# Performance work log

Measured on AMD Instinct MI355X. Metric: run time of the kernel, lower is better.

Reference implementation:

```python
import jax, jax.numpy as jnp
import numpy as np

BETA = 10.0    # ste surrogate-gradient scale (module default beta=10)
SLOPE = 1.0
GAMMA = 100.0  # trigger sharpness (module default gamma=100)
EPS = 1e-30

# Straight-through estimator: hard threshold forward, sigmoid-derivative surrogate backward
@jax.custom_vjp
def ste(v):
    return (v > 0).astype(v.dtype)

def _ste_fwd(v):
    return ste(v), v

def _ste_bwd(v, g):
    e = jnp.exp(-SLOPE * v)
    return (BETA * g * SLOPE * e / ((e + 1.0) ** 2 + EPS),)

ste.defvjp(_ste_fwd, _ste_bwd)


def setup_inputs() -> dict:
    key = jax.random.key(0)
    k1, k2, k3 = jax.random.split(key, 3)
    B, I, O = 256, 1024, 1024
    ACT_RATIO = 0.1
    x = jax.random.normal(k1, (B, I), dtype=jnp.float32)
    v_weight = jax.random.uniform(k2, (O, I), dtype=jnp.float32) - (1.0 - ACT_RATIO)
    # fc weight: xavier uniform
    bound = float(np.sqrt(6.0 / (I + O)))
    fc_weight = jax.random.uniform(k3, (O, I), dtype=jnp.float32, minval=-bound, maxval=bound)
    return {"x": x, "v_weight": v_weight, "fc_weight": fc_weight}


def reference(x, v_weight, fc_weight):
    # x: [B, I]; v_weight, fc_weight: [O, I]
    mask = ste(v_weight)                        # [O, I], 0/1 child mask
    x_en = x[:, None, :] * mask                 # [B, O, I] (x_enlarge * ste(v))
    w = fc_weight * mask                        # [O, I] masked matmul weight
    y = x @ w.T                                 # [B, O]
    # trigger value: tanh(gamma*|x|) where child, 1 where not; prod over input dim
    delta_en = jnp.tanh(GAMMA * jnp.abs(x_en)) * mask + (1.0 - mask)  # [B, O, I]
    delta = jnp.prod(delta_en, axis=-1)         # [B, O]
    y = jax.nn.relu(y * delta)
    return (y, delta)
```

## Files before the change

### kernel.cpp

```cpp
#include <hip/hip_runtime.h>
#include <cmath>

#define B_ 256
#define I_ 1024
#define O_ 1024

typedef __attribute__((ext_vector_type(8))) short short8;
typedef __attribute__((ext_vector_type(4))) float f32x4;

__device__ inline unsigned short f2bf(float f) {
  union { float f; unsigned u; } c;
  c.f = f;
  unsigned u = c.u;
  return (unsigned short)((u + 0x7FFFu + ((u >> 16) & 1u)) >> 16);
}

#define WBLKS ((O_ * I_) / 2048)
#define XBLKS ((B_ * I_) / 2048)

__global__ __launch_bounds__(256) void prep_all(
    const float* __restrict__ x, const float* __restrict__ vw,
    const float* __restrict__ fcw, unsigned short* __restrict__ xb,
    unsigned short* __restrict__ ltb, unsigned short* __restrict__ wb,
    unsigned short* __restrict__ mb) {
  const int bid = blockIdx.x;
  if (bid < WBLKS) {
    int idx = (bid * 256 + threadIdx.x) * 8;
    float4 v0 = *reinterpret_cast<const float4*>(vw + idx);
    float4 v1 = *reinterpret_cast<const float4*>(vw + idx + 4);
    float4 f0 = *reinterpret_cast<const float4*>(fcw + idx);
    float4 f1 = *reinterpret_cast<const float4*>(fcw + idx + 4);
    float va[8] = {v0.x, v0.y, v0.z, v0.w, v1.x, v1.y, v1.z, v1.w};
    float fa[8] = {f0.x, f0.y, f0.z, f0.w, f1.x, f1.y, f1.z, f1.w};
    short8 wv, mv;
#pragma unroll
    for (int j = 0; j < 8; ++j) {
      bool m = va[j] > 0.0f;
      wv[j] = (short)f2bf(m ? fa[j] : 0.0f);
      mv[j] = (short)(m ? 0x3F80 : 0x0000);
    }
    *reinterpret_cast<short8*>(wb + idx) = wv;
    *reinterpret_cast<short8*>(mb + idx) = mv;
  } else {
    int idx = ((bid - WBLKS) * 256 + threadIdx.x) * 8;
    float4 x0 = *reinterpret_cast<const float4*>(x + idx);
    float4 x1 = *reinterpret_cast<const float4*>(x + idx + 4);
    float xa[8] = {x0.x, x0.y, x0.z, x0.w, x1.x, x1.y, x1.z, x1.w};
    short8 xv, lv;
#pragma unroll
    for (int j = 0; j < 8; ++j) {
      xv[j] = (short)f2bf(xa[j]);
      float l = fmaxf(logf(tanhf(100.0f * fabsf(xa[j]))), -1e30f);
      lv[j] = (short)f2bf(l);
    }
    *reinterpret_cast<short8*>(xb + idx) = xv;
    *reinterpret_cast<short8*>(ltb + idx) = lv;
  }
}

__global__ __launch_bounds__(512) void mfma_fused2(
    const unsigned short* __restrict__ xb, const unsigned short* __restrict__ ltb,
    const unsigned short* __restrict__ wb, const unsigned short* __restrict__ mb,
    float* __restrict__ out) {
  const int on0 = blockIdx.x * 32;
  const int bm0 = blockIdx.y * 32;

  __shared__ short As[2][32][72];
  __shared__ short Ls[2][32][72];
  __shared__ short Ws[2][32][72];
  __shared__ short Ms[2][32][72];

  const int t = threadIdx.x;
  const int lane = t & 63;
  const int wid = t >> 6;
  const int kg = wid >> 2;
  const int wm = (wid >> 1) & 1, wn = wid & 1;
  const int lr = lane & 15;
  const int lk = (lane >> 4) * 8;

  const int tl = t & 255;
  const int srow = tl >> 3;
  const int scol = (tl & 7) * 8;

  const size_t aoff = (size_t)(bm0 + srow) * I_ + kg * 512 + scol;
  const size_t boff = (size_t)(on0 + srow) * I_ + kg * 512 + scol;

  short8 rx = *reinterpret_cast<const short8*>(xb + aoff);
  short8 rl = *reinterpret_cast<const short8*>(ltb + aoff);
  short8 rw = *reinterpret_cast<const short8*>(wb + boff);
  short8 rm = *reinterpret_cast<const short8*>(mb + boff);

  f32x4 accd = {0.f, 0.f, 0.f, 0.f};
  f32x4 accs = {0.f, 0.f, 0.f, 0.f};

  for (int kt = 0; kt < 512; kt += 64) {
    __syncthreads();
    *reinterpret_cast<short8*>(&As[kg][srow][scol]) = rx;
    *reinterpret_cast<short8*>(&Ls[kg][srow][scol]) = rl;
    *reinterpret_cast<short8*>(&Ws[kg][srow][scol]) = rw;
    *reinterpret_cast<short8*>(&Ms[kg][srow][scol]) = rm;
    if (kt + 64 < 512) {
      rx = *reinterpret_cast<const short8*>(xb + aoff + kt + 64);
      rl = *reinterpret_cast<const short8*>(ltb + aoff + kt + 64);
      rw = *reinterpret_cast<const short8*>(wb + boff + kt + 64);
      rm = *reinterpret_cast<const short8*>(mb + boff + kt + 64);
    }
    __syncthreads();
#pragma unroll
    for (int ks = 0; ks < 2; ++ks) {
      const int kb = ks * 32 + lk;
      short8 af = *reinterpret_cast<const short8*>(&As[kg][wm * 16 + lr][kb]);
      short8 lf = *reinterpret_cast<const short8*>(&Ls[kg][wm * 16 + lr][kb]);
      short8 wf = *reinterpret_cast<const short8*>(&Ws[kg][wn * 16 + lr][kb]);
      short8 mf = *reinterpret_cast<const short8*>(&Ms[kg][wn * 16 + lr][kb]);
      accd = __builtin_amdgcn_mfma_f32_16x16x32_bf16(af, wf, accd, 0, 0, 0);
      accs = __builtin_amdgcn_mfma_f32_16x16x32_bf16(lf, mf, accs, 0, 0, 0);
    }
  }

  __syncthreads();
  float* red = reinterpret_cast<float*>(&As[0][0][0]);
  const int ridx = ((wid & 3) * 64 + lane) * 8;
  if (kg == 1) {
#pragma unroll
    for (int r = 0; r < 4; ++r) {
      red[ridx + r] = accd[r];
      red[ridx + 4 + r] = accs[r];
    }
  }
  __syncthreads();
  if (kg == 0) {
    const int orow = bm0 + wm * 16 + (lane >> 4) * 4;
    const int ocol = on0 + wn * 16 + lr;
#pragma unroll
    for (int r = 0; r < 4; ++r) {
      float dsum = accd[r] + red[ridx + r];
      float ssum = accs[r] + red[ridx + 4 + r];
      float d = expf(ssum);
      float y = fmaxf(dsum * d, 0.0f);
      size_t off = (size_t)(orow + r) * O_ + ocol;
      out[off] = y;
      out[(size_t)B_ * O_ + off] = d;
    }
  }
}

__global__ __launch_bounds__(256) void dual_gemm_f32(
    const float* __restrict__ x, const float* __restrict__ vw,
    const float* __restrict__ fcw, float* __restrict__ out) {
  const int on0 = blockIdx.x * 64;
  const int bm0 = blockIdx.y * 64;
  __shared__ float xs[32][68];
  __shared__ float ls[32][68];
  __shared__ float wsm[32][68];
  __shared__ float msh[32][68];
  const int t = threadIdx.x;
  const int tx = t & 15, ty = t >> 4;
  const int m0 = ty * 4, n0 = tx * 4;
  float accd[4][4] = {{0.f}};
  float accs[4][4] = {{0.f}};
  for (int kt = 0; kt < I_; kt += 32) {
#pragma unroll
    for (int j = 0; j < 8; ++j) {
      int f = j * 256 + t;
      int m = f >> 5;
      int kk = f & 31;
      int gk = kt + kk;
      float xv = x[(size_t)(bm0 + m) * I_ + gk];
      xs[kk][m] = xv;
      ls[kk][m] = fmaxf(logf(tanhf(100.0f * fabsf(xv))), -1e30f);
      float vv = vw[(size_t)(on0 + m) * I_ + gk];
      float fv = fcw[(size_t)(on0 + m) * I_ + gk];
      float mk = vv > 0.0f ? 1.0f : 0.0f;
      wsm[kk][m] = fv * mk;
      msh[kk][m] = mk;
    }
    __syncthreads();
#pragma unroll
    for (int kk = 0; kk < 32; ++kk) {
      float4 xv = *reinterpret_cast<const float4*>(&xs[kk][m0]);
      float4 lv = *reinterpret_cast<const float4*>(&ls[kk][m0]);
      float4 wv = *reinterpret_cast<const float4*>(&wsm[kk][n0]);
      float4 mv = *reinterpret_cast<const float4*>(&msh[kk][n0]);
      float xa[4] = {xv.x, xv.y, xv.z, xv.w};
      float la[4] = {lv.x, lv.y, lv.z, lv.w};
      float wa[4] = {wv.x, wv.y, wv.z, wv.w};
      float ma[4] = {mv.x, mv.y, mv.z, mv.w};
#pragma unroll
      for (int i = 0; i < 4; ++i)
#pragma unroll
        for (int j = 0; j < 4; ++j) {
          accd[i][j] = fmaf(xa[i], wa[j], accd[i][j]);
          accs[i][j] = fmaf(la[i], ma[j], accs[i][j]);
        }
    }
    __syncthreads();
  }
#pragma unroll
  for (int i = 0; i < 4; ++i) {
    int row = bm0 + m0 + i;
#pragma unroll
    for (int j = 0; j < 4; ++j) {
      float delta = expf(accs[i][j]);
      out[(size_t)row * O_ + on0 + n0 + j] = fmaxf(accd[i][j] * delta, 0.0f);
      out[(size_t)B_ * O_ + (size_t)row * O_ + on0 + n0 + j] = delta;
    }
  }
}

extern "C" void kernel_launch(void* const* d_in, const int* in_sizes, int n_in,
                              void* d_out, int out_size, void* d_ws,
                              size_t ws_size, hipStream_t stream) {
  const float* x = (const float*)d_in[0];
  const float* vw = (const float*)d_in[1];
  const float* fcw = (const float*)d_in[2];
  float* out = (float*)d_out;

  const size_t xbB = (size_t)B_ * I_ * 2;
  const size_t wbB = (size_t)O_ * I_ * 2;
  const size_t bfB = 2 * xbB + 2 * wbB;

  unsigned short* xb = (unsigned short*)d_ws;
  unsigned short* ltb = (unsigned short*)((char*)d_ws + xbB);
  unsigned short* wb = (unsigned short*)((char*)d_ws + 2 * xbB);
  unsigned short* mb = (unsigned short*)((char*)d_ws + 2 * xbB + wbB);

  if (ws_size >= bfB) {
    prep_all<<<WBLKS + XBLKS, 256, 0, stream>>>(x, vw, fcw, xb, ltb, wb, mb);
    mfma_fused2<<<dim3(O_ / 32, B_ / 32), 512, 0, stream>>>(xb, ltb, wb, mb, out);
  } else {
    dual_gemm_f32<<<dim3(O_ / 64, B_ / 64, 1), 256, 0, stream>>>(x, vw, fcw, out);
  }
}
```

Before: 16.78 us.

## Fuse bf16 conversion prep into MFMA kernel and drop workspace pass

Removes the separate prep kernel that wrote bf16 copies of x, log-tanh(x), masked weights and mask to workspace. The MFMA kernel now loads fp32 inputs directly and does the conversion, log-tanh and masking in registers before staging to LDS. It also uses fast exp/log intrinsics and remaps block indices to group tiles. The goal is to save a kernel launch and a full round trip of the bf16 intermediates through memory. In exchange, x-derived transcendental work is redone by each of the 32 column blocks, and every block now reads twice as many fp32 bytes.

```diff
diff --git a/kernel.cpp b/kernel.cpp
--- a/kernel.cpp
+++ b/kernel.cpp
@@ -15,55 +15,21 @@
   return (unsigned short)((u + 0x7FFFu + ((u >> 16) & 1u)) >> 16);
 }
 
-#define WBLKS ((O_ * I_) / 2048)
-#define XBLKS ((B_ * I_) / 2048)
-
-__global__ __launch_bounds__(256) void prep_all(
-    const float* __restrict__ x, const float* __restrict__ vw,
-    const float* __restrict__ fcw, unsigned short* __restrict__ xb,
-    unsigned short* __restrict__ ltb, unsigned short* __restrict__ wb,
-    unsigned short* __restrict__ mb) {
-  const int bid = blockIdx.x;
-  if (bid < WBLKS) {
-    int idx = (bid * 256 + threadIdx.x) * 8;
-    float4 v0 = *reinterpret_cast<const float4*>(vw + idx);
-    float4 v1 = *reinterpret_cast<const float4*>(vw + idx + 4);
-    float4 f0 = *reinterpret_cast<const float4*>(fcw + idx);
-    float4 f1 = *reinterpret_cast<const float4*>(fcw + idx + 4);
-    float va[8] = {v0.x, v0.y, v0.z, v0.w, v1.x, v1.y, v1.z, v1.w};
-    float fa[8] = {f0.x, f0.y, f0.z, f0.w, f1.x, f1.y, f1.z, f1.w};
-    short8 wv, mv;
-#pragma unroll
-    for (int j = 0; j < 8; ++j) {
-      bool m = va[j] > 0.0f;
-      wv[j] = (short)f2bf(m ? fa[j] : 0.0f);
-      mv[j] = (short)(m ? 0x3F80 : 0x0000);
-    }
-    *reinterpret_cast<short8*>(wb + idx) = wv;
-    *reinterpret_cast<short8*>(mb + idx) = mv;
-  } else {
-    int idx = ((bid - WBLKS) * 256 + threadIdx.x) * 8;
-    float4 x0 = *reinterpret_cast<const float4*>(x + idx);
-    float4 x1 = *reinterpret_cast<const float4*>(x + idx + 4);
-    float xa[8] = {x0.x, x0.y, x0.z, x0.w, x1.x, x1.y, x1.z, x1.w};
-    short8 xv, lv;
-#pragma unroll
-    for (int j = 0; j < 8; ++j) {
-      xv[j] = (short)f2bf(xa[j]);
-      float l = fmaxf(logf(tanhf(100.0f * fabsf(xa[j]))), -1e30f);
-      lv[j] = (short)f2bf(l);
-    }
-    *reinterpret_cast<short8*>(xb + idx) = xv;
-    *reinterpret_cast<short8*>(ltb + idx) = lv;
-  }
+__device__ inline float fast_lt(float xv) {
+  float z = 100.0f * fabsf(xv);
+  float t = __expf(-2.0f * z);
+  float lt = __logf(1.0f - t) - __logf(1.0f + t);
+  return fmaxf(lt, -1e30f);
 }
 
-__global__ __launch_bounds__(512) void mfma_fused2(
-    const unsigned short* __restrict__ xb, const unsigned short* __restrict__ ltb,
-    const unsigned short* __restrict__ wb, const unsigned short* __restrict__ mb,
-    float* __restrict__ out) {
-  const int on0 = blockIdx.x * 32;
-  const int bm0 = blockIdx.y * 32;
+__global__ __launch_bounds__(512) void harsanyi_fused(
+    const float* __restrict__ x, const float* __restrict__ vw,
+    const float* __restrict__ fcw, float* __restrict__ out) {
+  const int bid = blockIdx.x;
+  const int cx = bid & 7, wi = bid >> 3;
+  const int nblk = (cx & 3) * 8 + (wi & 7);
+  const int mblk = (cx >> 2) * 4 + (wi >> 3);
+  const int on0 = nblk * 32, bm0 = mblk * 32;
 
   __shared__ short As[2][32][72];
   __shared__ short Ls[2][32][72];
@@ -82,44 +48,61 @@
   const int srow = tl >> 3;
   const int scol = (tl & 7) * 8;
 
-  const size_t aoff = (size_t)(bm0 + srow) * I_ + kg * 512 + scol;
-  const size_t boff = (size_t)(on0 + srow) * I_ + kg * 512 + scol;
+  const float* xp = x + (size_t)(bm0 + srow) * I_ + kg * 512 + scol;
+  const float* vp = vw + (size_t)(on0 + srow) * I_ + kg * 512 + scol;
+  const float* fp = fcw + (size_t)(on0 + srow) * I_ + kg * 512 + scol;
 
-  short8 rx = *reinterpret_cast<const short8*>(xb + aoff);
-  short8 rl = *reinterpret_cast<const short8*>(ltb + aoff);
-  short8 rw = *reinterpret_cast<const short8*>(wb + boff);
-  short8 rm = *reinterpret_cast<const short8*>(mb + boff);
+  float4 xa0 = *(const float4*)(xp);
+  float4 xa1 = *(const float4*)(xp + 4);
+  float4 va0 = *(const float4*)(vp);
+  float4 va1 = *(const float4*)(vp + 4);
+  float4 fa0 = *(const float4*)(fp);
+  float4 fa1 = *(const float4*)(fp + 4);
 
   f32x4 accd = {0.f, 0.f, 0.f, 0.f};
   f32x4 accs = {0.f, 0.f, 0.f, 0.f};
 
   for (int kt = 0; kt < 512; kt += 64) {
+    float xa[8] = {xa0.x, xa0.y, xa0.z, xa0.w, xa1.x, xa1.y, xa1.z, xa1.w};
+    float va[8] = {va0.x, va0.y, va0.z, va0.w, va1.x, va1.y, va1.z, va1.w};
+    float fa[8] = {fa0.x, fa0.y, fa0.z, fa0.w, fa1.x, fa1.y, fa1.z, fa1.w};
+    short8 xs_, ls_, ws_, ms_;
+#pragma unroll
+    for (int j = 0; j < 8; ++j) {
+      xs_[j] = (short)f2bf(xa[j]);
+      ls_[j] = (short)f2bf(fast_lt(xa[j]));
+      bool m = va[j] > 0.0f;
+      ws_[j] = m ? (short)f2bf(fa[j]) : (short)0;
+      ms_[j] = (short)(m ? 0x3F80 : 0x0000);
+    }
     __syncthreads();
-    *reinterpret_cast<short8*>(&As[kg][srow][scol]) = rx;
-    *reinterpret_cast<short8*>(&Ls[kg][srow][scol]) = rl;
-    *reinterpret_cast<short8*>(&Ws[kg][srow][scol]) = rw;
-    *reinterpret_cast<short8*>(&Ms[kg][srow][scol]) = rm;
+    *(short8*)(&As[kg][srow][scol]) = xs_;
+    *(short8*)(&Ls[kg][srow][scol]) = ls_;
+    *(short8*)(&Ws[kg][srow][scol]) = ws_;
+    *(short8*)(&Ms[kg][srow][scol]) = ms_;
     if (kt + 64 < 512) {
-      rx = *reinterpret_cast<const short8*>(xb + aoff + kt + 64);
-      rl = *reinterpret_cast<const short8*>(ltb + aoff + kt + 64);
-      rw = *reinterpret_cast<const short8*>(wb + boff + kt + 64);
-      rm = *reinterpret_cast<const short8*>(mb + boff + kt + 64);
+      xa0 = *(const float4*)(xp + kt + 64);
+      xa1 = *(const float4*)(xp + kt + 68);
+      va0 = *(const float4*)(vp + kt + 64);
+      va1 = *(const float4*)(vp + kt + 68);
+      fa0 = *(const float4*)(fp + kt + 64);
+      fa1 = *(const float4*)(fp + kt + 68);
     }
     __syncthreads();
 #pragma unroll
     for (int ks = 0; ks < 2; ++ks) {
       const int kb = ks * 32 + lk;
-      short8 af = *reinterpret_cast<const short8*>(&As[kg][wm * 16 + lr][kb]);
-      short8 lf = *reinterpret_cast<const short8*>(&Ls[kg][wm * 16 + lr][kb]);
-      short8 wf = *reinterpret_cast<const short8*>(&Ws[kg][wn * 16 + lr][kb]);
-      short8 mf = *reinterpret_cast<const short8*>(&Ms[kg][wn * 16 + lr][kb]);
+      short8 af = *(const short8*)(&As[kg][wm * 16 + lr][kb]);
+      short8 lf = *(const short8*)(&Ls[kg][wm * 16 + lr][kb]);
+      short8 wf = *(const short8*)(&Ws[kg][wn * 16 + lr][kb]);
+      short8 mf = *(const short8*)(&Ms[kg][wn * 16 + lr][kb]);
       accd = __builtin_amdgcn_mfma_f32_16x16x32_bf16(af, wf, accd, 0, 0, 0);
       accs = __builtin_amdgcn_mfma_f32_16x16x32_bf16(lf, mf, accs, 0, 0, 0);
     }
   }
 
   __syncthreads();
-  float* red = reinterpret_cast<float*>(&As[0][0][0]);
+  float* red = (float*)(&As[0][0][0]);
   const int ridx = ((wid & 3) * 64 + lane) * 8;
   if (kg == 1) {
 #pragma unroll
@@ -136,74 +119,11 @@
     for (int r = 0; r < 4; ++r) {
       float dsum = accd[r] + red[ridx + r];
       float ssum = accs[r] + red[ridx + 4 + r];
-      float d = expf(ssum);
+      float d = __expf(ssum);
       float y = fmaxf(dsum * d, 0.0f);
       size_t off = (size_t)(orow + r) * O_ + ocol;
       out[off] = y;
       out[(size_t)B_ * O_ + off] = d;
-    }
-  }
-}
-
-__global__ __launch_bounds__(256) void dual_gemm_f32(
-    const float* __restrict__ x, const float* __restrict__ vw,
-    const float* __restrict__ fcw, float* __restrict__ out) {
-  const int on0 = blockIdx.x * 64;
-  const int bm0 = blockIdx.y * 64;
-  __shared__ float xs[32][68];
-  __shared__ float ls[32][68];
-  __shared__ float wsm[32][68];
-  __shared__ float msh[32][68];
-  const int t = threadIdx.x;
-  const int tx = t & 15, ty = t >> 4;
-  const int m0 = ty * 4, n0 = tx * 4;
-  float accd[4][4] = {{0.f}};
-  float accs[4][4] = {{0.f}};
-  for (int kt = 0; kt < I_; kt += 32) {
-#pragma unroll
-    for (int j = 0; j < 8; ++j) {
-      int f = j * 256 + t;
-      int m = f >> 5;
-      int kk = f & 31;
-      int gk = kt + kk;
-      float xv = x[(size_t)(bm0 + m) * I_ + gk];
-      xs[kk][m] = xv;
-      ls[kk][m] = fmaxf(logf(tanhf(100.0f * fabsf(xv))), -1e30f);
-      float vv = vw[(size_t)(on0 + m) * I_ + gk];
-      float fv = fcw[(size_t)(on0 + m) * I_ + gk];
-      float mk = vv > 0.0f ? 1.0f : 0.0f;
-      wsm[kk][m] = fv * mk;
-      msh[kk][m] = mk;
-    }
-    __syncthreads();
-#pragma unroll
-    for (int kk = 0; kk < 32; ++kk) {
-      float4 xv = *reinterpret_cast<const float4*>(&xs[kk][m0]);
-      float4 lv = *reinterpret_cast<const float4*>(&ls[kk][m0]);
-      float4 wv = *reinterpret_cast<const float4*>(&wsm[kk][n0]);
-      float4 mv = *reinterpret_cast<const float4*>(&msh[kk][n0]);
-      float xa[4] = {xv.x, xv.y, xv.z, xv.w};
-      float la[4] = {lv.x, lv.y, lv.z, lv.w};
-      float wa[4] = {wv.x, wv.y, wv.z, wv.w};
-      float ma[4] = {mv.x, mv.y, mv.z, mv.w};
-#pragma unroll
-      for (int i = 0; i < 4; ++i)
-#pragma unroll
-        for (int j = 0; j < 4; ++j) {
-          accd[i][j] = fmaf(xa[i], wa[j], accd[i][j]);
-          accs[i][j] = fmaf(la[i], ma[j], accs[i][j]);
-        }
-    }
-    __syncthreads();
-  }
-#pragma unroll
-  for (int i = 0; i < 4; ++i) {
-    int row = bm0 + m0 + i;
-#pragma unroll
-    for (int j = 0; j < 4; ++j) {
-      float delta = expf(accs[i][j]);
-      out[(size_t)row * O_ + on0 + n0 + j] = fmaxf(accd[i][j] * delta, 0.0f);
-      out[(size_t)B_ * O_ + (size_t)row * O_ + on0 + n0 + j] = delta;
     }
   }
 }
@@ -216,19 +136,5 @@
   const float* fcw = (const float*)d_in[2];
   float* out = (float*)d_out;
 
-  const size_t xbB = (size_t)B_ * I_ * 2;
-  const size_t wbB = (size_t)O_ * I_ * 2;
-  const size_t bfB = 2 * xbB + 2 * wbB;
-
-  unsigned short* xb = (unsigned short*)d_ws;
-  unsigned short* ltb = (unsigned short*)((char*)d_ws + xbB);
-  unsigned short* wb = (unsigned short*)((char*)d_ws + 2 * xbB);
-  unsigned short* mb = (unsigned short*)((char*)d_ws + 2 * xbB + wbB);
-
-  if (ws_size >= bfB) {
-    prep_all<<<WBLKS + XBLKS, 256, 0, stream>>>(x, vw, fcw, xb, ltb, wb, mb);
-    mfma_fused2<<<dim3(O_ / 32, B_ / 32), 512, 0, stream>>>(xb, ltb, wb, mb, out);
-  } else {
-    dual_gemm_f32<<<dim3(O_ / 64, B_ / 64, 1), 256, 0, stream>>>(x, vw, fcw, out);
-  }
+  harsanyi_fused<<<256, 512, 0, stream>>>(x, vw, fcw, out);
 }
```

Result: slower. 20.56 us (+22.6%).

## Merge prep and MFMA GEMM into one cooperative kernel with grid sync

Applied to the files above, without the earlier changes.

Replaces the two launches (bf16 prep pass, then fused MFMA dual GEMM) with a single cooperative kernel of 256 blocks. Each block converts its slice of the weights and activations, then waits at a grid-wide barrier before running the same GEMM tile schedule. The log-tanh and exp calls are also swapped for fast intrinsics. The aim is to remove one launch gap and the tail between the kernels. In exchange the kernel relies on a grid barrier and co-residency of all 256 blocks, and the fast transcendentals are slightly less accurate.

```diff
diff --git a/kernel.cpp b/kernel.cpp
--- a/kernel.cpp
+++ b/kernel.cpp
@@ -1,4 +1,5 @@
 #include <hip/hip_runtime.h>
+#include <hip/hip_cooperative_groups.h>
 #include <cmath>
 
 #define B_ 256
@@ -8,24 +9,30 @@
 typedef __attribute__((ext_vector_type(8))) short short8;
 typedef __attribute__((ext_vector_type(4))) float f32x4;
 
-__device__ inline unsigned short f2bf(float f) {
+__device__ inline unsigned f2bf(float f) {
   union { float f; unsigned u; } c;
   c.f = f;
   unsigned u = c.u;
-  return (unsigned short)((u + 0x7FFFu + ((u >> 16) & 1u)) >> 16);
-}
-
-#define WBLKS ((O_ * I_) / 2048)
-#define XBLKS ((B_ * I_) / 2048)
-
-__global__ __launch_bounds__(256) void prep_all(
+  return (u + 0x7FFFu + ((u >> 16) & 1u)) >> 16;
+}
+
+__device__ inline float fast_lt(float xv) {
+  float z = 100.0f * fabsf(xv);
+  float t = __expf(-2.0f * z);
+  float lt = __logf((1.0f - t) / (1.0f + t));
+  return fmaxf(lt, -1e30f);
+}
+
+__global__ __launch_bounds__(512) void harsanyi_coop(
     const float* __restrict__ x, const float* __restrict__ vw,
     const float* __restrict__ fcw, unsigned short* __restrict__ xb,
     unsigned short* __restrict__ ltb, unsigned short* __restrict__ wb,
-    unsigned short* __restrict__ mb) {
+    unsigned short* __restrict__ mb, float* __restrict__ out) {
+  const int t = threadIdx.x;
   const int bid = blockIdx.x;
-  if (bid < WBLKS) {
-    int idx = (bid * 256 + threadIdx.x) * 8;
+
+  {
+    size_t idx = ((size_t)bid * 512 + t) * 8;
     float4 v0 = *reinterpret_cast<const float4*>(vw + idx);
     float4 v1 = *reinterpret_cast<const float4*>(vw + idx + 4);
     float4 f0 = *reinterpret_cast<const float4*>(fcw + idx);
@@ -36,13 +43,14 @@
 #pragma unroll
     for (int j = 0; j < 8; ++j) {
       bool m = va[j] > 0.0f;
-      wv[j] = (short)f2bf(m ? fa[j] : 0.0f);
+      wv[j] = m ? (short)f2bf(fa[j]) : (short)0;
       mv[j] = (short)(m ? 0x3F80 : 0x0000);
     }
     *reinterpret_cast<short8*>(wb + idx) = wv;
     *reinterpret_cast<short8*>(mb + idx) = mv;
-  } else {
-    int idx = ((bid - WBLKS) * 256 + threadIdx.x) * 8;
+  }
+  if (t < 128) {
+    size_t idx = ((size_t)bid * 128 + t) * 8;
     float4 x0 = *reinterpret_cast<const float4*>(x + idx);
     float4 x1 = *reinterpret_cast<const float4*>(x + idx + 4);
     float xa[8] = {x0.x, x0.y, x0.z, x0.w, x1.x, x1.y, x1.z, x1.w};
@@ -50,27 +58,22 @@
 #pragma unroll
     for (int j = 0; j < 8; ++j) {
       xv[j] = (short)f2bf(xa[j]);
-      float l = fmaxf(logf(tanhf(100.0f * fabsf(xa[j]))), -1e30f);
-      lv[j] = (short)f2bf(l);
+      lv[j] = (short)f2bf(fast_lt(xa[j]));
     }
     *reinterpret_cast<short8*>(xb + idx) = xv;
     *reinterpret_cast<short8*>(ltb + idx) = lv;
   }
-}
-
-__global__ __launch_bounds__(512) void mfma_fused2(
-    const unsigned short* __restrict__ xb, const unsigned short* __restrict__ ltb,
-    const unsigned short* __restrict__ wb, const unsigned short* __restrict__ mb,
-    float* __restrict__ out) {
-  const int on0 = blockIdx.x * 32;
-  const int bm0 = blockIdx.y * 32;
+
+  cooperative_groups::this_grid().sync();
+
+  const int on0 = (bid & 31) * 32;
+  const int bm0 = (bid >> 5) * 32;
 
   __shared__ short As[2][32][72];
   __shared__ short Ls[2][32][72];
   __shared__ short Ws[2][32][72];
   __shared__ short Ms[2][32][72];
 
-  const int t = threadIdx.x;
   const int lane = t & 63;
   const int wid = t >> 6;
   const int kg = wid >> 2;
@@ -136,7 +139,7 @@
     for (int r = 0; r < 4; ++r) {
       float dsum = accd[r] + red[ridx + r];
       float ssum = accs[r] + red[ridx + 4 + r];
-      float d = expf(ssum);
+      float d = __expf(ssum);
       float y = fmaxf(dsum * d, 0.0f);
       size_t off = (size_t)(orow + r) * O_ + ocol;
       out[off] = y;
@@ -168,7 +171,7 @@
       int gk = kt + kk;
       float xv = x[(size_t)(bm0 + m) * I_ + gk];
       xs[kk][m] = xv;
-      ls[kk][m] = fmaxf(logf(tanhf(100.0f * fabsf(xv))), -1e30f);
+      ls[kk][m] = fast_lt(xv);
       float vv = vw[(size_t)(on0 + m) * I_ + gk];
       float fv = fcw[(size_t)(on0 + m) * I_ + gk];
       float mk = vv > 0.0f ? 1.0f : 0.0f;
@@ -189,9 +192,9 @@
 #pragma unroll
       for (int i = 0; i < 4; ++i)
 #pragma unroll
-        for (int j = 0; j < 4; ++j) {
-          accd[i][j] = fmaf(xa[i], wa[j], accd[i][j]);
-          accs[i][j] = fmaf(la[i], ma[j], accs[i][j]);
+        for (int jj = 0; jj < 4; ++jj) {
+          accd[i][jj] = fmaf(xa[i], wa[jj], accd[i][jj]);
+          accs[i][jj] = fmaf(la[i], ma[jj], accs[i][jj]);
         }
     }
     __syncthreads();
@@ -200,10 +203,10 @@
   for (int i = 0; i < 4; ++i) {
     int row = bm0 + m0 + i;
 #pragma unroll
-    for (int j = 0; j < 4; ++j) {
-      float delta = expf(accs[i][j]);
-      out[(size_t)row * O_ + on0 + n0 + j] = fmaxf(accd[i][j] * delta, 0.0f);
-      out[(size_t)B_ * O_ + (size_t)row * O_ + on0 + n0 + j] = delta;
+    for (int jj = 0; jj < 4; ++jj) {
+      float delta = __expf(accs[i][jj]);
+      out[(size_t)row * O_ + on0 + n0 + jj] = fmaxf(accd[i][jj] * delta, 0.0f);
+      out[(size_t)B_ * O_ + (size_t)row * O_ + on0 + n0 + jj] = delta;
     }
   }
 }
@@ -226,8 +229,10 @@
   unsigned short* mb = (unsigned short*)((char*)d_ws + 2 * xbB + wbB);
 
   if (ws_size >= bfB) {
-    prep_all<<<WBLKS + XBLKS, 256, 0, stream>>>(x, vw, fcw, xb, ltb, wb, mb);
-    mfma_fused2<<<dim3(O_ / 32, B_ / 32), 512, 0, stream>>>(xb, ltb, wb, mb, out);
+    void* args[] = {(void*)&x, (void*)&vw, (void*)&fcw, (void*)&xb,
+                    (void*)&ltb, (void*)&wb, (void*)&mb, (void*)&out};
+    hipLaunchCooperativeKernel((const void*)harsanyi_coop, dim3(256), dim3(512),
+                               args, 0, stream);
   } else {
     dual_gemm_f32<<<dim3(O_ / 64, B_ / 64, 1), 256, 0, stream>>>(x, vw, fcw, out);
   }
```

Result: slower. 51.12 us (+204.7%).
